# Optimization experiments

Measured on AMD Instinct MI355X. Metric: run time of the kernel, lower is better.

Reference implementation:

```python
import jax, jax.numpy as jnp
import numpy as np

HIDDEN = 512
LATENT = 256
NUM_NODE_TYPES = 16


def setup_inputs() -> dict:
    key = jax.random.key(0)
    ks = jax.random.split(key, 9)
    s = lambda fan_in: 1.0 / np.sqrt(fan_in)
    return {
        "z": jax.random.normal(ks[0], (1024, LATENT), dtype=jnp.float32),
        "num_nodes": 128,
        "W_z": jax.random.uniform(ks[1], (LATENT, HIDDEN), jnp.float32, -s(LATENT), s(LATENT)),
        "b_z": jax.random.uniform(ks[2], (HIDDEN,), jnp.float32, -s(LATENT), s(LATENT)),
        "W_node": jax.random.uniform(ks[3], (HIDDEN, NUM_NODE_TYPES), jnp.float32, -s(HIDDEN), s(HIDDEN)),
        "b_node": jax.random.uniform(ks[4], (NUM_NODE_TYPES,), jnp.float32, -s(HIDDEN), s(HIDDEN)),
        "W_e1": jax.random.uniform(ks[5], (2 * HIDDEN, HIDDEN), jnp.float32, -s(2 * HIDDEN), s(2 * HIDDEN)),
        "b_e1": jax.random.uniform(ks[6], (HIDDEN,), jnp.float32, -s(2 * HIDDEN), s(2 * HIDDEN)),
        "W_e2": jax.random.uniform(ks[7], (HIDDEN, 1), jnp.float32, -s(HIDDEN), s(HIDDEN)),
        "b_e2": jax.random.uniform(ks[8], (1,), jnp.float32, -s(HIDDEN), s(HIDDEN)),
    }


def reference(z, num_nodes, W_z, b_z, W_node, b_node, W_e1, b_e1, W_e2, b_e2):
    # h: [B, H]
    h = jax.nn.relu(z @ W_z + b_z)
    B = z.shape[0]
    # h_expanded: [B, N, H] (same h replicated per node, as in the original)
    h_expanded = jnp.broadcast_to(h[:, None, :], (B, num_nodes, h.shape[-1]))
    node_logits = h_expanded @ W_node + b_node  # [B, N, T]
    # Every (i, j) pair in the original loop uses cat(h, h) -> identical scalar per batch.
    h_pair = jnp.concatenate([h, h], axis=-1)  # [B, 2H]
    p = jax.nn.sigmoid(jax.nn.relu(h_pair @ W_e1 + b_e1) @ W_e2 + b_e2)  # [B, 1]
    # Scatter onto strict lower triangle (j < i), zeros elsewhere.
    tril = jnp.tril(jnp.ones((num_nodes, num_nodes), dtype=z.dtype), k=-1)  # [N, N]
    edge_probs = p[:, :, None] * tril[None, :, :]  # [B, N, N]
    return node_logits, edge_probs
```

## Files before the change

kernel.cpp:

```cpp
#include <hip/hip_runtime.h>
#include <hip/hip_bf16.h>
#include <math.h>

#define BB 1024
#define LL 256
#define HH 512
#define TT 16
#define NN 128

#define NODE_F4 (BB * NN * TT / 4)
#define EDGE_F4 (BB * NN * NN / 4)

typedef short bf16x8 __attribute__((ext_vector_type(8)));
typedef float f32x4  __attribute__((ext_vector_type(4)));

static __device__ __forceinline__ short bfbits(float f) {
    __hip_bfloat16 h = __float2bfloat16(f);
    return *reinterpret_cast<short*>(&h);
}

static __device__ __forceinline__ int h_addr(int row, int col) {
    return (row << 10) + ((((col >> 3) ^ (row & 7)) << 4)) + ((col & 7) << 1);
}

__device__ __forceinline__ void transpose_tile(const float* __restrict__ in,
                                               __hip_bfloat16* __restrict__ out,
                                               int k0, int n0, int Kdim, bool fold,
                                               __hip_bfloat16 (*tile)[34]) {
    const int tx = threadIdx.x & 31;
    const int ty = threadIdx.x >> 5;
    #pragma unroll
    for (int r = ty; r < 32; r += 8) {
        float v = in[(k0 + r) * HH + n0 + tx];
        if (fold) v += in[(k0 + r + HH) * HH + n0 + tx];
        tile[r][tx] = __float2bfloat16(v);
    }
    __syncthreads();
    #pragma unroll
    for (int r = ty; r < 32; r += 8) {
        out[(n0 + r) * Kdim + k0 + tx] = tile[tx][r];
    }
}

__global__ __launch_bounds__(256) void k_prep(const float* __restrict__ Wz,
                                              const float* __restrict__ We1,
                                              const float* __restrict__ Wn,
                                              __hip_bfloat16* __restrict__ WzT,
                                              __hip_bfloat16* __restrict__ WsumT,
                                              __hip_bfloat16* __restrict__ WnT) {
    __shared__ __hip_bfloat16 tile[32][34];
    const int bid = blockIdx.x;
    const int tid = threadIdx.x;
    if (bid < 128) {
        transpose_tile(Wz, WzT, (bid >> 4) * 32, (bid & 15) * 32, LL, false, tile);
    } else if (bid < 384) {
        const int t = bid - 128;
        transpose_tile(We1, WsumT, (t >> 4) * 32, (t & 15) * 32, HH, true, tile);
    } else {
        const int u = (bid - 384) * 256 + tid;
        WnT[u] = __float2bfloat16(Wn[(u & 511) * TT + (u >> 9)]);
    }
}

__global__ __launch_bounds__(512) void k_mega(const float* __restrict__ z,
                                              const __hip_bfloat16* __restrict__ WzT,
                                              const __hip_bfloat16* __restrict__ WsumT,
                                              const __hip_bfloat16* __restrict__ WnT,
                                              const float* __restrict__ bz,
                                              const float* __restrict__ be1,
                                              const float* __restrict__ We2,
                                              const float* __restrict__ bn,
                                              const float* __restrict__ be2,
                                              f32x4* __restrict__ out) {
    __shared__ char  hbuf[16384];
    __shared__ f32x4 nod_lds[8][64];
    __shared__ float pw_lds[8][16];
    __shared__ float nodef[16][16];
    __shared__ float pfin[16];

    const int tid  = threadIdx.x;
    const int w    = tid >> 6;
    const int lane = tid & 63;
    const int l16  = lane & 15, quad = lane >> 4;
    const int g = blockIdx.x >> 2, q = blockIdx.x & 3;
    const int r0 = g << 4;

    {
        bf16x8 afr[8];
        const float4* zf = (const float4*)(z + (r0 + l16) * LL);
        #pragma unroll
        for (int kt = 0; kt < 8; ++kt) {
            float4 v0 = zf[quad * 2 + kt * 8];
            float4 v1 = zf[quad * 2 + kt * 8 + 1];
            bf16x8 a;
            a[0] = bfbits(v0.x); a[1] = bfbits(v0.y); a[2] = bfbits(v0.z); a[3] = bfbits(v0.w);
            a[4] = bfbits(v1.x); a[5] = bfbits(v1.y); a[6] = bfbits(v1.z); a[7] = bfbits(v1.w);
            afr[kt] = a;
        }
        #pragma unroll
        for (int i = 0; i < 4; ++i) {
            const int nt = (w << 2) + i;
            const short* Bp = (const short*)WzT + (nt * 16 + l16) * LL + quad * 8;
            f32x4 acc = {0.f, 0.f, 0.f, 0.f};
            #pragma unroll
            for (int kt = 0; kt < 8; ++kt) {
                bf16x8 b = *(const bf16x8*)(Bp + kt * 32);
                acc = __builtin_amdgcn_mfma_f32_16x16x32_bf16(afr[kt], b, acc, 0, 0, 0);
            }
            const int col = nt * 16 + l16;
            const float bb = bz[col];
            #pragma unroll
            for (int r = 0; r < 4; ++r) {
                float hv = fmaxf(acc[r] + bb, 0.f);
                *(short*)(hbuf + h_addr(quad * 4 + r, col)) = bfbits(hv);
            }
        }
    }
    __syncthreads();

    {
        f32x4 acc = {0.f, 0.f, 0.f, 0.f};
        const short* Bp = (const short*)WnT + l16 * HH + quad * 8;
        #pragma unroll
        for (int kk = 0; kk < 2; ++kk) {
            const int kt = w * 2 + kk;
            bf16x8 a = *(const bf16x8*)(hbuf + h_addr(l16, quad * 8 + kt * 32));
            bf16x8 b = *(const bf16x8*)(Bp + kt * 32);
            acc = __builtin_amdgcn_mfma_f32_16x16x32_bf16(a, b, acc, 0, 0, 0);
        }
        nod_lds[w][lane] = acc;
    }

    {
        f32x4 acc[4];
        #pragma unroll
        for (int i = 0; i < 4; ++i) acc[i] = (f32x4){0.f, 0.f, 0.f, 0.f};
        #pragma unroll
        for (int kt = 0; kt < 16; ++kt) {
            bf16x8 a = *(const bf16x8*)(hbuf + h_addr(l16, quad * 8 + kt * 32));
            #pragma unroll
            for (int i = 0; i < 4; ++i) {
                const int nt = (w << 2) + i;
                bf16x8 b = *(const bf16x8*)((const short*)WsumT +
                            (nt * 16 + l16) * HH + quad * 8 + kt * 32);
                acc[i] = __builtin_amdgcn_mfma_f32_16x16x32_bf16(a, b, acc[i], 0, 0, 0);
            }
        }
        float psum[4] = {0.f, 0.f, 0.f, 0.f};
        #pragma unroll
        for (int i = 0; i < 4; ++i) {
            const int col = ((w << 2) + i) * 16 + l16;
            const float bb = be1[col], w2 = We2[col];
            float sr[4];
            #pragma unroll
            for (int r = 0; r < 4; ++r) sr[r] = fmaxf(acc[i][r] + bb, 0.f) * w2;
            #pragma unroll
            for (int off = 1; off < 16; off <<= 1) {
                #pragma unroll
                for (int r = 0; r < 4; ++r) sr[r] += __shfl_xor(sr[r], off);
            }
            #pragma unroll
            for (int r = 0; r < 4; ++r) psum[r] += sr[r];
        }
        if (l16 == 0) {
            #pragma unroll
            for (int r = 0; r < 4; ++r) pw_lds[w][quad * 4 + r] = psum[r];
        }
    }
    __syncthreads();

    if (w == 0) {
        f32x4 s = nod_lds[0][lane];
        #pragma unroll
        for (int ww = 1; ww < 8; ++ww) {
            f32x4 t = nod_lds[ww][lane];
            s[0] += t[0]; s[1] += t[1]; s[2] += t[2]; s[3] += t[3];
        }
        const float bb = bn[l16];
        #pragma unroll
        for (int r = 0; r < 4; ++r)
            nodef[quad * 4 + r][l16] = s[r] + bb;
    }
    if (w == 1 && lane < 16) {
        float t = 0.f;
        #pragma unroll
        for (int ww = 0; ww < 8; ++ww) t += pw_lds[ww][lane];
        pfin[lane] = 1.f / (1.f + expf(-(t + be2[0])));
    }
    __syncthreads();

    {
        const f32x4* nf4 = (const f32x4*)nodef;
        #pragma unroll
        for (int i = 0; i < 4; ++i) {
            const int idx = i * 512 + tid;
            const int bl  = idx >> 7;
            const int rem = idx & 127;
            const int nl  = rem >> 2;
            const int t4  = rem & 3;
            __builtin_nontemporal_store(nf4[bl * 4 + t4],
                out + (r0 + bl) * 512 + (q * 32 + nl) * 4 + t4);
        }
    }

    {
        f32x4* oedge = out + NODE_F4;
        #pragma unroll
        for (int i = 0; i < 4; ++i) {
            const int b = r0 + (q << 2) + i;
            const float pv = pfin[(q << 2) + i];
            #pragma unroll
            for (int it = 0; it < 8; ++it) {
                const int e  = it * 512 + tid;
                const int ii = e >> 5;
                const int j0 = (e & 31) << 2;
                f32x4 v;
                v[0] = (j0 + 0 < ii) ? pv : 0.f;
                v[1] = (j0 + 1 < ii) ? pv : 0.f;
                v[2] = (j0 + 2 < ii) ? pv : 0.f;
                v[3] = (j0 + 3 < ii) ? pv : 0.f;
                __builtin_nontemporal_store(v, oedge + b * 4096 + e);
            }
        }
    }
}

extern "C" void kernel_launch(void* const* d_in, const int* in_sizes, int n_in,
                              void* d_out, int out_size, void* d_ws, size_t ws_size,
                              hipStream_t stream) {
    const float* z    = (const float*)d_in[0];
    const float* Wz   = (const float*)d_in[2];
    const float* bz   = (const float*)d_in[3];
    const float* Wn   = (const float*)d_in[4];
    const float* bn   = (const float*)d_in[5];
    const float* We1  = (const float*)d_in[6];
    const float* be1  = (const float*)d_in[7];
    const float* We2  = (const float*)d_in[8];
    const float* be2  = (const float*)d_in[9];
    float* out = (float*)d_out;

    char* base = (char*)d_ws;
    __hip_bfloat16* WzT    = (__hip_bfloat16*)(base);
    __hip_bfloat16* WsumT  = (__hip_bfloat16*)(base +  256 * 1024);
    __hip_bfloat16* WnT    = (__hip_bfloat16*)(base +  768 * 1024);

    k_prep<<<416, 256, 0, stream>>>(Wz, We1, Wn, WzT, WsumT, WnT);

    k_mega<<<256, 512, 0, stream>>>(z, WzT, WsumT, WnT,
                                    bz, be1, We2, bn, be2, (f32x4*)out);

    (void)in_sizes; (void)n_in; (void)out_size; (void)ws_size;
}
```

Before: 134.3 us.

## Split edge-MLP columns across the four blocks of each group with atomic reduction

Each of the four blocks sharing a 16-row group previously computed the full 512-column edge hidden layer redundantly. Now each block computes only its quarter of the columns and atomically adds its partial dot product into a workspace. A per-group counter plus spin-wait synchronises the four blocks before the sigmoid. The kernel is launched cooperatively so all blocks are co-resident and the spin cannot deadlock. This cuts the MFMA and weight-load work in that stage to a quarter, at the cost of global atomics, a spin barrier and an extra zeroing block in the prep kernel.

```diff
diff --git a/kernel.cpp b/kernel.cpp
--- a/kernel.cpp
+++ b/kernel.cpp
@@ -47,7 +47,9 @@
                                               const float* __restrict__ Wn,
                                               __hip_bfloat16* __restrict__ WzT,
                                               __hip_bfloat16* __restrict__ WsumT,
-                                              __hip_bfloat16* __restrict__ WnT) {
+                                              __hip_bfloat16* __restrict__ WnT,
+                                              float* __restrict__ p_acc,
+                                              int* __restrict__ grp_cnt) {
     __shared__ __hip_bfloat16 tile[32][34];
     const int bid = blockIdx.x;
     const int tid = threadIdx.x;
@@ -56,13 +58,16 @@
     } else if (bid < 384) {
         const int t = bid - 128;
         transpose_tile(We1, WsumT, (t >> 4) * 32, (t & 15) * 32, HH, true, tile);
-    } else {
+    } else if (bid < 416) {
         const int u = (bid - 384) * 256 + tid;
         WnT[u] = __float2bfloat16(Wn[(u & 511) * TT + (u >> 9)]);
-    }
-}
-
-__global__ __launch_bounds__(512) void k_mega(const float* __restrict__ z,
+    } else {
+        if (tid < 256) ((float4*)p_acc)[tid] = make_float4(0.f, 0.f, 0.f, 0.f);
+        if (tid < 16)  ((int4*)grp_cnt)[tid] = make_int4(0, 0, 0, 0);
+    }
+}
+
+__global__ __launch_bounds__(512) void k_main(const float* __restrict__ z,
                                               const __hip_bfloat16* __restrict__ WzT,
                                               const __hip_bfloat16* __restrict__ WsumT,
                                               const __hip_bfloat16* __restrict__ WnT,
@@ -71,12 +76,14 @@
                                               const float* __restrict__ We2,
                                               const float* __restrict__ bn,
                                               const float* __restrict__ be2,
+                                              float* __restrict__ p_acc,
+                                              int* __restrict__ grp_cnt,
                                               f32x4* __restrict__ out) {
     __shared__ char  hbuf[16384];
     __shared__ f32x4 nod_lds[8][64];
     __shared__ float pw_lds[8][16];
     __shared__ float nodef[16][16];
-    __shared__ float pfin[16];
+    __shared__ float pfin[4];
 
     const int tid  = threadIdx.x;
     const int w    = tid >> 6;
@@ -132,39 +139,28 @@
     }
 
     {
-        f32x4 acc[4];
-        #pragma unroll
-        for (int i = 0; i < 4; ++i) acc[i] = (f32x4){0.f, 0.f, 0.f, 0.f};
+        const int nt = q * 8 + w;
+        const short* Bp = (const short*)WsumT + (nt * 16 + l16) * HH + quad * 8;
+        f32x4 acc = {0.f, 0.f, 0.f, 0.f};
         #pragma unroll
         for (int kt = 0; kt < 16; ++kt) {
             bf16x8 a = *(const bf16x8*)(hbuf + h_addr(l16, quad * 8 + kt * 32));
-            #pragma unroll
-            for (int i = 0; i < 4; ++i) {
-                const int nt = (w << 2) + i;
-                bf16x8 b = *(const bf16x8*)((const short*)WsumT +
-                            (nt * 16 + l16) * HH + quad * 8 + kt * 32);
-                acc[i] = __builtin_amdgcn_mfma_f32_16x16x32_bf16(a, b, acc[i], 0, 0, 0);
-            }
-        }
-        float psum[4] = {0.f, 0.f, 0.f, 0.f};
-        #pragma unroll
-        for (int i = 0; i < 4; ++i) {
-            const int col = ((w << 2) + i) * 16 + l16;
-            const float bb = be1[col], w2 = We2[col];
-            float sr[4];
-            #pragma unroll
-            for (int r = 0; r < 4; ++r) sr[r] = fmaxf(acc[i][r] + bb, 0.f) * w2;
-            #pragma unroll
-            for (int off = 1; off < 16; off <<= 1) {
-                #pragma unroll
-                for (int r = 0; r < 4; ++r) sr[r] += __shfl_xor(sr[r], off);
-            }
-            #pragma unroll
-            for (int r = 0; r < 4; ++r) psum[r] += sr[r];
+            bf16x8 b = *(const bf16x8*)(Bp + kt * 32);
+            acc = __builtin_amdgcn_mfma_f32_16x16x32_bf16(a, b, acc, 0, 0, 0);
+        }
+        const int col = nt * 16 + l16;
+        const float bb = be1[col], w2 = We2[col];
+        float sr[4];
+        #pragma unroll
+        for (int r = 0; r < 4; ++r) sr[r] = fmaxf(acc[r] + bb, 0.f) * w2;
+        #pragma unroll
+        for (int off = 1; off < 16; off <<= 1) {
+            #pragma unroll
+            for (int r = 0; r < 4; ++r) sr[r] += __shfl_xor(sr[r], off);
         }
         if (l16 == 0) {
             #pragma unroll
-            for (int r = 0; r < 4; ++r) pw_lds[w][quad * 4 + r] = psum[r];
+            for (int r = 0; r < 4; ++r) pw_lds[w][quad * 4 + r] = sr[r];
         }
     }
     __syncthreads();
@@ -185,9 +181,14 @@
         float t = 0.f;
         #pragma unroll
         for (int ww = 0; ww < 8; ++ww) t += pw_lds[ww][lane];
-        pfin[lane] = 1.f / (1.f + expf(-(t + be2[0])));
-    }
-    __syncthreads();
+        atomicAdd(p_acc + r0 + lane, t);
+        __threadfence();
+    }
+    __syncthreads();
+
+    if (tid == 0)
+        __hip_atomic_fetch_add(grp_cnt + g, 1, __ATOMIC_RELEASE,
+                               __HIP_MEMORY_SCOPE_AGENT);
 
     {
         const f32x4* nf4 = (const f32x4*)nodef;
@@ -203,12 +204,24 @@
         }
     }
 
+    if (tid == 0) {
+        while (__hip_atomic_load(grp_cnt + g, __ATOMIC_ACQUIRE,
+                                 __HIP_MEMORY_SCOPE_AGENT) < 4) { }
+    }
+    __syncthreads();
+    if (tid < 4) {
+        float t = __hip_atomic_load(p_acc + r0 + (q << 2) + tid,
+                                    __ATOMIC_RELAXED, __HIP_MEMORY_SCOPE_AGENT);
+        pfin[tid] = 1.f / (1.f + expf(-(t + be2[0])));
+    }
+    __syncthreads();
+
     {
         f32x4* oedge = out + NODE_F4;
         #pragma unroll
         for (int i = 0; i < 4; ++i) {
             const int b = r0 + (q << 2) + i;
-            const float pv = pfin[(q << 2) + i];
+            const float pv = pfin[i];
             #pragma unroll
             for (int it = 0; it < 8; ++it) {
                 const int e  = it * 512 + tid;
@@ -243,11 +256,20 @@
     __hip_bfloat16* WzT    = (__hip_bfloat16*)(base);
     __hip_bfloat16* WsumT  = (__hip_bfloat16*)(base +  256 * 1024);
     __hip_bfloat16* WnT    = (__hip_bfloat16*)(base +  768 * 1024);
-
-    k_prep<<<416, 256, 0, stream>>>(Wz, We1, Wn, WzT, WsumT, WnT);
-
-    k_mega<<<256, 512, 0, stream>>>(z, WzT, WsumT, WnT,
-                                    bz, be1, We2, bn, be2, (f32x4*)out);
+    float*          p_acc  = (float*)(base + 784 * 1024);
+    int*            grpcnt = (int*)(base + 788 * 1024);
+
+    k_prep<<<417, 256, 0, stream>>>(Wz, We1, Wn, WzT, WsumT, WnT, p_acc, grpcnt);
+
+    {
+        f32x4* outv = (f32x4*)out;
+        void* args[] = { (void*)&z, (void*)&WzT, (void*)&WsumT, (void*)&WnT,
+                         (void*)&bz, (void*)&be1, (void*)&We2, (void*)&bn,
+                         (void*)&be2, (void*)&p_acc, (void*)&grpcnt,
+                         (void*)&outv };
+        hipLaunchCooperativeKernel((const void*)k_main, dim3(256), dim3(512),
+                                   args, 0, stream);
+    }
 
     (void)in_sizes; (void)n_in; (void)out_size; (void)ws_size;
 }
```

Result: slower. 165.2 us (+23.1%).
